# Performance work log

Measured on AMD Instinct MI355X. Metric: run time of the kernel, lower is better.

Reference implementation:

```python
import jax, jax.numpy as jnp
import numpy as np

OUT_F, IN_F = 8192, 8192
RATIO = 0.05


def setup_inputs() -> dict:
    rng = np.random.default_rng(0)
    # Simulate the quantization performed in OrthoLinear.__init__ with numpy.
    w = (rng.standard_normal((OUT_F, IN_F)) * 0.02).astype(np.float32)
    w_abs = np.abs(w)
    k_idx = min(int(IN_F * 0.995), IN_F - 1)
    # torch.kthvalue(k) = k-th smallest (1-indexed) -> partition index k-1
    robust_max = np.partition(w_abs, k_idx - 1, axis=1)[:, k_idx - 1][:, None]
    robust_max = np.maximum(robust_max, 1e-6)
    scales = (robust_max / 7.0).astype(np.float32)
    w_int = np.clip(np.round(w / scales), -7, 7).astype(np.float32)
    resid = w - w_int * scales
    # top-k |residual| entries form the sparse CSR correction
    k = max(int(resid.size * RATIO), 1)
    metric = np.abs(resid).ravel()
    idx = np.argpartition(metric, -k)[-k:]
    idx.sort()
    rows = idx // IN_F
    cols = (idx % IN_F).astype(np.int32)
    vals = resid.ravel()[idx].astype(np.float16)
    ptr = np.zeros(OUT_F + 1, np.int32)
    ptr[1:] = np.cumsum(np.bincount(rows, minlength=OUT_F)).astype(np.int32)
    # pack two int4 (offset by +8) per byte: even cols -> low nibble, odd -> high
    offs = (w_int + 8.0).astype(np.uint8)
    packed = (offs[:, 0::2] | (offs[:, 1::2] << 4)).astype(np.int32)
    x = jax.random.normal(jax.random.key(0), (4, 8, IN_F), jnp.float32)
    return {
        "x": x,
        "base_packed": jnp.asarray(packed),
        "scales": jnp.asarray(scales.reshape(-1)),
        "ortho_vals": jnp.asarray(vals),
        "ortho_indices": jnp.asarray(cols),
        "ortho_ptr": jnp.asarray(ptr),
        "alpha": jnp.float32(1.0),
    }


def reference(x, base_packed, scales, ortho_vals, ortho_indices, ortho_ptr, alpha):
    lead = x.shape[:-1]
    in_f = x.shape[-1]
    out_f = base_packed.shape[0]
    xf = x.reshape(-1, in_f).astype(jnp.float32)  # [N, in]
    # dequantize packed int4 base weight: interleave low/high nibbles
    low = base_packed & 0xF
    high = (base_packed >> 4) & 0xF
    w_int = jnp.stack([low, high], axis=-1).reshape(out_f, in_f).astype(jnp.float32) - 8.0
    w_base = w_int * scales[:, None]  # [out, in]
    # CSR residual -> scatter into dense [out, in] (disjoint coords), then GEMM
    nnz = ortho_vals.shape[0]
    row_ids = jnp.searchsorted(ortho_ptr, jnp.arange(nnz, dtype=jnp.int32), side="right") - 1
    w_res = jnp.zeros((out_f, in_f), jnp.float32).at[row_ids, ortho_indices].add(
        ortho_vals.astype(jnp.float32)
    )
    out = xf @ w_base.T + alpha * (xf @ w_res.T)  # [N, out]
    return out.reshape(lead + (out_f,))
```

## Files before the change

### kernel.cpp

```cpp
#include <hip/hip_runtime.h>


#define IN_F 8192
#define OUT_F 8192
#define NROW 32
#define KSPLIT 8
#define KSEG (IN_F / KSPLIT)
#define CHUNKS (KSEG / 32)

typedef __attribute__((ext_vector_type(8))) short short8v;
typedef __attribute__((ext_vector_type(4))) float f32x4;

union Frag {
  int4 v;
  unsigned int u[4];
  short8v s;
};

__device__ __forceinline__ unsigned int cvt_pk_bf16(float lo, float hi) {
  unsigned int r;
  asm("v_cvt_pk_bf16_f32 %0, %1, %2" : "=v"(r) : "v"(lo), "v"(hi));
  return r;
}

__device__ __forceinline__ unsigned short f2bf(float f) {
  unsigned int u = __float_as_uint(f);
  u += 0x7FFFu + ((u >> 16) & 1u);
  return (unsigned short)(u >> 16);
}

__global__ __launch_bounds__(256) void prep_kernel(
    const float* __restrict__ x, unsigned short* __restrict__ x_hi,
    unsigned short* __restrict__ x_lo, unsigned short* __restrict__ xTb,
    float* __restrict__ out) {
  __shared__ unsigned short T[64 * 33];
  int tid = threadIdx.x;
  int k0 = blockIdx.x * 64;

  {
    float4 z = {0.f, 0.f, 0.f, 0.f};
    float4* o4 = (float4*)out;
    o4[blockIdx.x * 512 + tid] = z;
    o4[blockIdx.x * 512 + 256 + tid] = z;
  }

  int kk = tid & 63;
  int ng = tid >> 6;
#pragma unroll
  for (int p = 0; p < 8; ++p) {
    int n = p * 4 + ng;
    int idx = n * IN_F + k0 + kk;
    float v = x[idx];
    unsigned short h = f2bf(v);
    float hf = __uint_as_float((unsigned int)h << 16);
    unsigned short l = f2bf(v - hf);
    x_hi[idx] = h;
    x_lo[idx] = l;
    T[kk * 33 + n] = h;
  }
  __syncthreads();
  int kr = tid >> 2, q = tid & 3;
  unsigned int s0 = T[kr * 33 + q * 8 + 0], s1 = T[kr * 33 + q * 8 + 1];
  unsigned int s2 = T[kr * 33 + q * 8 + 2], s3 = T[kr * 33 + q * 8 + 3];
  unsigned int s4 = T[kr * 33 + q * 8 + 4], s5 = T[kr * 33 + q * 8 + 5];
  unsigned int s6 = T[kr * 33 + q * 8 + 6], s7 = T[kr * 33 + q * 8 + 7];
  int4 wv;
  wv.x = (int)(s0 | (s1 << 16));
  wv.y = (int)(s2 | (s3 << 16));
  wv.z = (int)(s4 | (s5 << 16));
  wv.w = (int)(s6 | (s7 << 16));
  ((int4*)xTb)[(size_t)(k0 + kr) * 4 + q] = wv;
}

__global__ __launch_bounds__(256) void fused_kernel(
    const int* __restrict__ packed, const float* __restrict__ scales,
    const float* __restrict__ vals, const int* __restrict__ cols,
    const int* __restrict__ rptr, const float* __restrict__ alphap,
    const unsigned short* __restrict__ x_hi,
    const unsigned short* __restrict__ x_lo,
    const unsigned short* __restrict__ xTb, float* __restrict__ out) {
  __shared__ float red[4][64 * 33];
  int tid = threadIdx.x;
  int lane = tid & 63;
  int w = tid >> 6;
  int og = blockIdx.x >> 3;
  int g = blockIdx.x & 7;
  int lo16 = lane & 15;
  int lhi = lane >> 4;

  int o = og * 64 + w * 16 + lo16;
  int kbeg = g * KSEG;
  const int4* wp = (const int4*)(packed + (size_t)o * (IN_F / 2) + (kbeg >> 1)) + lhi;
  const unsigned short* xh = x_hi + lo16 * IN_F + kbeg + 8 * lhi;
  const unsigned short* xl = x_lo + lo16 * IN_F + kbeg + 8 * lhi;

  f32x4 acc0 = {0.f, 0.f, 0.f, 0.f};
  f32x4 acc1 = {0.f, 0.f, 0.f, 0.f};

  Frag wA, h0A, l0A, h1A, l1A;
  Frag wB, h0B, l0B, h1B, l1B;

#define LOADIN(W_, H0, L0, H1, L1, c)                  \
  W_.v = wp[(c) * 4];                                  \
  H0.v = *(const int4*)(xh + (c) * 32);                \
  L0.v = *(const int4*)(xl + (c) * 32);                \
  H1.v = *(const int4*)(xh + 16 * IN_F + (c) * 32);    \
  L1.v = *(const int4*)(xl + 16 * IN_F + (c) * 32);

#define COMPUTE(W_, H0, L0, H1, L1)                                               \
  {                                                                               \
    Frag b;                                                                       \
    b.u[0] = cvt_pk_bf16((float)(W_.v.x & 15) - 8.0f, (float)(W_.v.x >> 4) - 8.0f); \
    b.u[1] = cvt_pk_bf16((float)(W_.v.y & 15) - 8.0f, (float)(W_.v.y >> 4) - 8.0f); \
    b.u[2] = cvt_pk_bf16((float)(W_.v.z & 15) - 8.0f, (float)(W_.v.z >> 4) - 8.0f); \
    b.u[3] = cvt_pk_bf16((float)(W_.v.w & 15) - 8.0f, (float)(W_.v.w >> 4) - 8.0f); \
    acc0 = __builtin_amdgcn_mfma_f32_16x16x32_bf16(H0.s, b.s, acc0, 0, 0, 0);     \
    acc0 = __builtin_amdgcn_mfma_f32_16x16x32_bf16(L0.s, b.s, acc0, 0, 0, 0);     \
    acc1 = __builtin_amdgcn_mfma_f32_16x16x32_bf16(H1.s, b.s, acc1, 0, 0, 0);     \
    acc1 = __builtin_amdgcn_mfma_f32_16x16x32_bf16(L1.s, b.s, acc1, 0, 0, 0);     \
  }

  LOADIN(wA, h0A, l0A, h1A, l1A, 0)
  for (int c = 0; c < CHUNKS; c += 2) {
    LOADIN(wB, h0B, l0B, h1B, l1B, c + 1)
    COMPUTE(wA, h0A, l0A, h1A, l1A)
    if (c + 2 < CHUNKS) {
      LOADIN(wA, h0A, l0A, h1A, l1A, c + 2)
    }
    COMPUTE(wB, h0B, l0B, h1B, l1B)
  }
#undef LOADIN
#undef COMPUTE

  float sc = scales[o];
#pragma unroll
  for (int r = 0; r < 4; ++r) {
    int m = lhi * 4 + r;
    atomicAdd(&out[(size_t)m * OUT_F + o], sc * acc0[r]);
    atomicAdd(&out[(size_t)(m + 16) * OUT_F + o], sc * acc1[r]);
  }

  float alpha = alphap[0];
  float* R = red[w];
#pragma unroll 1
  for (int rr = 0; rr < 2; ++rr) {
    int ro = og * 64 + g * 8 + w * 2 + rr;
    int js = rptr[ro], je = rptr[ro + 1];
    float acc[32];
#pragma unroll
    for (int i = 0; i < 32; ++i) acc[i] = 0.f;

    int j = js + lane;
    float vc = 0.f;
    int cc = 0;
    if (j < je) { vc = vals[j]; cc = cols[j]; }
    while (j < je) {
      int jn = j + 64;
      float vn = 0.f;
      int cn = 0;
      if (jn < je) { vn = vals[jn]; cn = cols[jn]; }
      const int4* xp = (const int4*)(xTb + (size_t)cc * NROW);
      int4 q0 = xp[0], q1 = xp[1], q2 = xp[2], q3 = xp[3];
#define UNP(dw, base)                                                          \
  {                                                                            \
    unsigned int ud = (unsigned int)(dw);                                      \
    acc[base] = fmaf(vc, __uint_as_float(ud << 16), acc[base]);                \
    acc[base + 1] = fmaf(vc, __uint_as_float(ud & 0xFFFF0000u), acc[base + 1]); \
  }
      UNP(q0.x, 0) UNP(q0.y, 2) UNP(q0.z, 4) UNP(q0.w, 6)
      UNP(q1.x, 8) UNP(q1.y, 10) UNP(q1.z, 12) UNP(q1.w, 14)
      UNP(q2.x, 16) UNP(q2.y, 18) UNP(q2.z, 20) UNP(q2.w, 22)
      UNP(q3.x, 24) UNP(q3.y, 26) UNP(q3.z, 28) UNP(q3.w, 30)
#undef UNP
      j = jn;
      vc = vn;
      cc = cn;
    }
#pragma unroll
    for (int i = 0; i < 32; ++i) R[lane * 33 + i] = acc[i];
    int cidx = lane & 31;
    int h = lane >> 5;
    float sum = 0.f;
#pragma unroll
    for (int r2 = 0; r2 < 32; ++r2) sum += R[(h * 32 + r2) * 33 + cidx];
    sum += __shfl_xor(sum, 32, 64);
    if (lane < 32) atomicAdd(&out[(size_t)lane * OUT_F + ro], alpha * sum);
  }
}

extern "C" void kernel_launch(void* const* d_in, const int* in_sizes, int n_in,
                              void* d_out, int out_size, void* d_ws, size_t ws_size,
                              hipStream_t stream) {
  const float* x = (const float*)d_in[0];
  const int* packed = (const int*)d_in[1];
  const float* scales = (const float*)d_in[2];
  const float* vals = (const float*)d_in[3];
  const int* cols = (const int*)d_in[4];
  const int* rptr = (const int*)d_in[5];
  const float* alphap = (const float*)d_in[6];
  float* out = (float*)d_out;

  unsigned short* x_hi = (unsigned short*)d_ws;
  unsigned short* x_lo = x_hi + NROW * IN_F;
  unsigned short* xTb = x_lo + NROW * IN_F;

  prep_kernel<<<IN_F / 64, 256, 0, stream>>>(x, x_hi, x_lo, xTb, out);
  fused_kernel<<<(OUT_F / 64) * KSPLIT, 256, 0, stream>>>(
      packed, scales, vals, cols, rptr, alphap, x_hi, x_lo, xTb, out);
}
```

Measured before the change: 300.6 us.

## Split fused kernel into dense, sparse, and reduce passes with partial buffers

Splits the fused dense+sparse kernel into separate dense MFMA and CSR sparse kernels. Both now write partial results into per-K-split slices of a workspace buffer instead of using atomicAdd. A final reduction kernel sums the nine slices into the output, and the output zeroing moves out of the prep kernel. Dropping the large shared reduction buffer from the dense kernel and adding launch_bounds(256,4) aims for higher occupancy and no atomic contention. The cost is two extra launches and about 9 MB of partial-buffer traffic.

```diff
diff --git a/kernel.cpp b/kernel.cpp
--- a/kernel.cpp
+++ b/kernel.cpp
@@ -7,6 +7,7 @@
 #define KSPLIT 8
 #define KSEG (IN_F / KSPLIT)
 #define CHUNKS (KSEG / 32)
+#define SLICE (NROW * OUT_F)
 
 typedef __attribute__((ext_vector_type(8))) short short8v;
 typedef __attribute__((ext_vector_type(4))) float f32x4;
@@ -31,19 +32,10 @@
 
 __global__ __launch_bounds__(256) void prep_kernel(
     const float* __restrict__ x, unsigned short* __restrict__ x_hi,
-    unsigned short* __restrict__ x_lo, unsigned short* __restrict__ xTb,
-    float* __restrict__ out) {
+    unsigned short* __restrict__ x_lo, unsigned short* __restrict__ xTb) {
   __shared__ unsigned short T[64 * 33];
   int tid = threadIdx.x;
   int k0 = blockIdx.x * 64;
-
-  {
-    float4 z = {0.f, 0.f, 0.f, 0.f};
-    float4* o4 = (float4*)out;
-    o4[blockIdx.x * 512 + tid] = z;
-    o4[blockIdx.x * 512 + 256 + tid] = z;
-  }
-
   int kk = tid & 63;
   int ng = tid >> 6;
 #pragma unroll
@@ -72,14 +64,10 @@
   ((int4*)xTb)[(size_t)(k0 + kr) * 4 + q] = wv;
 }
 
-__global__ __launch_bounds__(256) void fused_kernel(
+__global__ __launch_bounds__(256, 4) void dense_kernel(
     const int* __restrict__ packed, const float* __restrict__ scales,
-    const float* __restrict__ vals, const int* __restrict__ cols,
-    const int* __restrict__ rptr, const float* __restrict__ alphap,
     const unsigned short* __restrict__ x_hi,
-    const unsigned short* __restrict__ x_lo,
-    const unsigned short* __restrict__ xTb, float* __restrict__ out) {
-  __shared__ float red[4][64 * 33];
+    const unsigned short* __restrict__ x_lo, float* __restrict__ part) {
   int tid = threadIdx.x;
   int lane = tid & 63;
   int w = tid >> 6;
@@ -133,18 +121,28 @@
 #undef COMPUTE
 
   float sc = scales[o];
+  float* ps = part + (size_t)g * SLICE;
 #pragma unroll
   for (int r = 0; r < 4; ++r) {
     int m = lhi * 4 + r;
-    atomicAdd(&out[(size_t)m * OUT_F + o], sc * acc0[r]);
-    atomicAdd(&out[(size_t)(m + 16) * OUT_F + o], sc * acc1[r]);
-  }
-
+    ps[(size_t)m * OUT_F + o] = sc * acc0[r];
+    ps[(size_t)(m + 16) * OUT_F + o] = sc * acc1[r];
+  }
+}
+
+__global__ __launch_bounds__(256) void sparse_kernel(
+    const float* __restrict__ vals, const int* __restrict__ cols,
+    const int* __restrict__ rptr, const float* __restrict__ alphap,
+    const unsigned short* __restrict__ xTb, float* __restrict__ part8) {
+  __shared__ float red[4][64 * 33];
+  int tid = threadIdx.x;
+  int lane = tid & 63;
+  int w = tid >> 6;
   float alpha = alphap[0];
   float* R = red[w];
 #pragma unroll 1
   for (int rr = 0; rr < 2; ++rr) {
-    int ro = og * 64 + g * 8 + w * 2 + rr;
+    int ro = blockIdx.x * 8 + w * 2 + rr;
     int js = rptr[ro], je = rptr[ro + 1];
     float acc[32];
 #pragma unroll
@@ -184,8 +182,21 @@
 #pragma unroll
     for (int r2 = 0; r2 < 32; ++r2) sum += R[(h * 32 + r2) * 33 + cidx];
     sum += __shfl_xor(sum, 32, 64);
-    if (lane < 32) atomicAdd(&out[(size_t)lane * OUT_F + ro], alpha * sum);
-  }
+    if (lane < 32) part8[(size_t)lane * OUT_F + ro] = alpha * sum;
+  }
+}
+
+__global__ __launch_bounds__(256) void reduce_kernel(
+    const float* __restrict__ part, float* __restrict__ out) {
+  int i = blockIdx.x * 256 + threadIdx.x;
+  const float4* p4 = (const float4*)part;
+  float4 s = p4[i];
+#pragma unroll
+  for (int sl = 1; sl < 9; ++sl) {
+    float4 t = p4[i + sl * (SLICE / 4)];
+    s.x += t.x; s.y += t.y; s.z += t.z; s.w += t.w;
+  }
+  ((float4*)out)[i] = s;
 }
 
 extern "C" void kernel_launch(void* const* d_in, const int* in_sizes, int n_in,
@@ -203,8 +214,12 @@
   unsigned short* x_hi = (unsigned short*)d_ws;
   unsigned short* x_lo = x_hi + NROW * IN_F;
   unsigned short* xTb = x_lo + NROW * IN_F;
-
-  prep_kernel<<<IN_F / 64, 256, 0, stream>>>(x, x_hi, x_lo, xTb, out);
-  fused_kernel<<<(OUT_F / 64) * KSPLIT, 256, 0, stream>>>(
-      packed, scales, vals, cols, rptr, alphap, x_hi, x_lo, xTb, out);
-}
+  float* part = (float*)(xTb + NROW * IN_F);
+
+  prep_kernel<<<IN_F / 64, 256, 0, stream>>>(x, x_hi, x_lo, xTb);
+  dense_kernel<<<(OUT_F / 64) * KSPLIT, 256, 0, stream>>>(
+      packed, scales, x_hi, x_lo, part);
+  sparse_kernel<<<OUT_F / 8, 256, 0, stream>>>(
+      vals, cols, rptr, alphap, xTb, part + (size_t)8 * SLICE);
+  reduce_kernel<<<(SLICE / 4) / 256, 256, 0, stream>>>(part, out);
+}
```

After: 305.3 us. About the same (+1.5%).
